# Performance work log

Hardware: AMD Instinct MI355X
Metric: run time of the kernel (lower is better)

Reference implementation:

```python
import jax, jax.numpy as jnp
import numpy as np


def setup_inputs() -> dict:
    key = jax.random.key(0)
    k_x, k_w1, k_w2 = jax.random.split(key, 3)
    b, d, m, h = 256, 2048, 64, 128  # batch, d_model, history_length, d_out
    lim1 = 1.0 / np.sqrt(m + h)
    lim2 = 1.0 / np.sqrt(h + d)
    x = jax.random.normal(k_x, (b, d, m), dtype=jnp.float32)
    w1 = jax.random.uniform(k_w1, (m, h, d), dtype=jnp.float32, minval=-lim1, maxval=lim1)
    b1 = jnp.zeros((1, h, d), dtype=jnp.float32)
    w2 = jax.random.uniform(k_w2, (h, d), dtype=jnp.float32, minval=-lim2, maxval=lim2)
    b2 = jnp.zeros((1, h), dtype=jnp.float32)
    return {"x": x, "w1": w1, "b1": b1, "w2": w2, "b2": b2}


def reference(x, w1, b1, w2, b2):
    # per-neuron (per-d) MLP: contract over history m, then over hidden h
    hidden = jnp.einsum('bdm,mhd->bhd', x, w1) + b1  # (b, h, d)
    out = jnp.einsum('bhd,hd->bh', hidden, w2) + b2  # (b, h)
    return out
```

## Files before the change

### kernel.cpp

```cpp
#include <hip/hip_runtime.h>

typedef unsigned short u16;
typedef __attribute__((ext_vector_type(8))) short short8;
typedef __attribute__((ext_vector_type(4))) float f32x4;

#define D_TOT 2048
#define M_TOT 64
#define H_TOT 128
#define B_TOT 256
#define NG    256
#define XB    131072
#define W1M   262144

__device__ __forceinline__ u16 f2bf(float f) {
  unsigned u = __builtin_bit_cast(unsigned, f);
  u = (u + 0x7fffu + ((u >> 16) & 1u)) >> 16;
  return (u16)u;
}
__device__ __forceinline__ float bf2f(u16 v) {
  unsigned u = ((unsigned)v) << 16;
  return __builtin_bit_cast(float, u);
}

__global__ __launch_bounds__(256)
void nlm_p0(const float* __restrict__ b1, const float* __restrict__ w2,
            const float* __restrict__ b2, float* __restrict__ ch) {
  const int h = blockIdx.x, t = threadIdx.x;
  const float4* pb = (const float4*)(b1 + (size_t)h * D_TOT);
  const float4* pw = (const float4*)(w2 + (size_t)h * D_TOT);
  float s = 0.f;
  for (int i = t; i < D_TOT / 4; i += 256) {
    float4 a = pb[i], w = pw[i];
    s += a.x * w.x + a.y * w.y + a.z * w.z + a.w * w.w;
  }
  __shared__ float red[256];
  red[t] = s;
  __syncthreads();
  for (int off = 128; off > 0; off >>= 1) {
    if (t < off) red[t] += red[t + off];
    __syncthreads();
  }
  if (t == 0) ch[h] = red[0] + b2[h];
}

__global__ __launch_bounds__(256)
void nlm_pw(const float* __restrict__ w1, const float* __restrict__ w2,
            u16* __restrict__ Bp) {
  const int gq  = blockIdx.x & 63;
  const int hb  = blockIdx.x >> 6;
  const int dq0 = gq * 32;
  const int t   = threadIdx.x;
  __shared__ u16 tile[32 * 16 * 64];

#pragma unroll
  for (int rep = 0; rep < 4; ++rep) {
    const int tau = rep * 256 + t;
    const int h_l = tau >> 6, m = tau & 63;
    const int h   = hb * 16 + h_l;
    const float* w1p = w1 + (size_t)m * W1M + (size_t)h * D_TOT + dq0;
    const float* w2p = w2 + (size_t)h * D_TOT + dq0;
    u16* dst = tile + h_l * 64 + m;
#pragma unroll
    for (int q = 0; q < 8; ++q) {
      float4 a = *(const float4*)(w1p + q * 4);
      float4 s = *(const float4*)(w2p + q * 4);
      dst[(q * 4 + 0) * 1024] = f2bf(a.x * s.x);
      dst[(q * 4 + 1) * 1024] = f2bf(a.y * s.y);
      dst[(q * 4 + 2) * 1024] = f2bf(a.z * s.z);
      dst[(q * 4 + 3) * 1024] = f2bf(a.w * s.w);
    }
  }
  __syncthreads();
#pragma unroll 4
  for (int dc = 0; dc < 32; ++dc) {
    const int g = gq * 4 + (dc >> 3), c = dc & 7;
    u16* out = Bp + (((size_t)g * 8 + c) * H_TOT + hb * 16) * 64 + t * 4;
    *(ushort4*)out = *(const ushort4*)(tile + dc * 1024 + t * 4);
  }
}

__global__ __launch_bounds__(512, 4)
void nlm_p1(const float* __restrict__ x, const u16* __restrict__ Bp,
            u16* __restrict__ partial) {
  __shared__ __align__(16) u16 As[64 * 72];
  __shared__ __align__(16) u16 Bs[128 * 72];

  const int tid  = threadIdx.x;
  const int g    = blockIdx.x & 255;
  const int bq   = blockIdx.x >> 8;
  const int d0   = g * 8;
  const int lane = tid & 63, wave = tid >> 6;
  const int wm   = wave >> 2;
  const int wn   = wave & 3;
  const int quad = lane >> 4, l16 = lane & 15;

  const int a_bl = tid >> 3, a_p = tid & 7;
  const float* xrow = x + (size_t)(bq * 64 + a_bl) * XB
                        + (size_t)d0 * M_TOT + a_p * 8;
  const int b_h = tid >> 2, b_qp = tid & 3;
  const u16* bsrc = Bp + ((size_t)g * 8 * H_TOT + b_h) * 64 + b_qp * 16;

  f32x4 acc[2][2];
#pragma unroll
  for (int i = 0; i < 2; ++i)
#pragma unroll
    for (int j = 0; j < 2; ++j) acc[i][j] = (f32x4){0.f, 0.f, 0.f, 0.f};

  for (int c = 0; c < 8; ++c) {
    {
      const float* xp = xrow + c * M_TOT;
      float4 v0 = *(const float4*)(xp);
      float4 v1 = *(const float4*)(xp + 4);
      short8 av;
      av[0] = (short)f2bf(v0.x); av[1] = (short)f2bf(v0.y);
      av[2] = (short)f2bf(v0.z); av[3] = (short)f2bf(v0.w);
      av[4] = (short)f2bf(v1.x); av[5] = (short)f2bf(v1.y);
      av[6] = (short)f2bf(v1.z); av[7] = (short)f2bf(v1.w);
      *(short8*)(As + a_bl * 72 + a_p * 8) = av;
    }
    {
      const u16* bp = bsrc + (size_t)c * (H_TOT * 64);
      *(short8*)(Bs + b_h * 72 + b_qp * 16)     = *(const short8*)(bp);
      *(short8*)(Bs + b_h * 72 + b_qp * 16 + 8) = *(const short8*)(bp + 8);
    }
    __syncthreads();
#pragma unroll
    for (int s = 0; s < 2; ++s) {
      short8 af[2], bf[2];
#pragma unroll
      for (int i = 0; i < 2; ++i)
        af[i] = *(const short8*)(As + (wm * 32 + i * 16 + l16) * 72 + s * 32 + quad * 8);
#pragma unroll
      for (int j = 0; j < 2; ++j)
        bf[j] = *(const short8*)(Bs + (wn * 32 + j * 16 + l16) * 72 + s * 32 + quad * 8);
#pragma unroll
      for (int i = 0; i < 2; ++i)
#pragma unroll
        for (int j = 0; j < 2; ++j)
          acc[i][j] = __builtin_amdgcn_mfma_f32_16x16x32_bf16(af[i], bf[j], acc[i][j], 0, 0, 0);
    }
    __syncthreads();
  }

#pragma unroll
  for (int i = 0; i < 2; ++i)
#pragma unroll
    for (int j = 0; j < 2; ++j) {
      const int hcol = wn * 32 + j * 16 + l16;
#pragma unroll
      for (int r = 0; r < 4; ++r) {
        const int brow = bq * 64 + wm * 32 + i * 16 + quad * 4 + r;
        partial[((size_t)brow * NG + g) * H_TOT + hcol] = f2bf(acc[i][j][r]);
      }
    }
}

__global__ __launch_bounds__(256)
void nlm_p2(const u16* __restrict__ partial, const float* __restrict__ ch,
            float* __restrict__ out) {
  const int b = blockIdx.x, t = threadIdx.x;
  const int h2   = t & 63;
  const int half = t >> 6;
  const u16* base = partial + ((size_t)b * NG + half * 64) * H_TOT + 2 * h2;
  float s0 = 0.f, s1 = 0.f;
#pragma unroll 8
  for (int gg = 0; gg < 64; ++gg) {
    unsigned v = __builtin_nontemporal_load((const unsigned*)(base + (size_t)gg * H_TOT));
    s0 += bf2f((u16)(v & 0xffffu));
    s1 += bf2f((u16)(v >> 16));
  }
  __shared__ float red0[256], red1[256];
  red0[t] = s0;
  red1[t] = s1;
  __syncthreads();
  if (t < 64) {
    float a0 = red0[t] + red0[t + 64] + red0[t + 128] + red0[t + 192];
    float a1 = red1[t] + red1[t + 64] + red1[t + 128] + red1[t + 192];
    out[(size_t)b * H_TOT + 2 * t]     = a0 + ch[2 * t];
    out[(size_t)b * H_TOT + 2 * t + 1] = a1 + ch[2 * t + 1];
  }
}

extern "C" void kernel_launch(void* const* d_in, const int* in_sizes, int n_in,
                              void* d_out, int out_size, void* d_ws, size_t ws_size,
                              hipStream_t stream) {
  const float* x  = (const float*)d_in[0];
  const float* w1 = (const float*)d_in[1];
  const float* b1 = (const float*)d_in[2];
  const float* w2 = (const float*)d_in[3];
  const float* b2 = (const float*)d_in[4];
  float* out = (float*)d_out;

  u16*   partial = (u16*)d_ws;
  u16*   Bp      = (u16*)((char*)d_ws + (size_t)B_TOT * NG * H_TOT * sizeof(u16));
  float* ch      = (float*)((char*)d_ws + (size_t)B_TOT * NG * H_TOT * sizeof(u16)
                                        + (size_t)NG * 8 * H_TOT * 64 * sizeof(u16));

  nlm_p0<<<dim3(128),  dim3(256), 0, stream>>>(b1, w2, b2, ch);
  nlm_pw<<<dim3(512),  dim3(256), 0, stream>>>(w1, w2, Bp);
  nlm_p1<<<dim3(1024), dim3(512), 0, stream>>>(x, Bp, partial);
  nlm_p2<<<dim3(256),  dim3(256), 0, stream>>>(partial, ch, out);
}
```

Before: 266.8 us.

## Double-group d per block and prefetch next chunk into registers

Each p1 block now covers 16 d-values instead of 8, which halves the grid and halves the bf16 partial-sum buffer written by p1 and read back by p2. The global loads for the next chunk of x and Bp are issued into registers right after the barrier, so they overlap with the MFMA work on the current chunk. The Bp layout is simplified to a flat per-d index. The cost is fewer blocks (512) to fill the GPU and more registers held live per thread.

Measured after the change: 273.9 us. 2.6% more time.

```diff
diff --git a/kernel.cpp b/kernel.cpp
--- a/kernel.cpp
+++ b/kernel.cpp
@@ -8,7 +8,7 @@
 #define M_TOT 64
 #define H_TOT 128
 #define B_TOT 256
-#define NG    256
+#define NGRP  128
 #define XB    131072
 #define W1M   262144
 
@@ -73,8 +73,8 @@
   __syncthreads();
 #pragma unroll 4
   for (int dc = 0; dc < 32; ++dc) {
-    const int g = gq * 4 + (dc >> 3), c = dc & 7;
-    u16* out = Bp + (((size_t)g * 8 + c) * H_TOT + hb * 16) * 64 + t * 4;
+    const int dg = dq0 + dc;
+    u16* out = Bp + ((size_t)dg * H_TOT + hb * 16) * 64 + t * 4;
     *(ushort4*)out = *(const ushort4*)(tile + dc * 1024 + t * 4);
   }
 }
@@ -86,9 +86,9 @@
   __shared__ __align__(16) u16 Bs[128 * 72];
 
   const int tid  = threadIdx.x;
-  const int g    = blockIdx.x & 255;
-  const int bq   = blockIdx.x >> 8;
-  const int d0   = g * 8;
+  const int G    = blockIdx.x & 127;
+  const int bq   = blockIdx.x >> 7;
+  const int dg0  = G * 16;
   const int lane = tid & 63, wave = tid >> 6;
   const int wm   = wave >> 2;
   const int wn   = wave & 3;
@@ -96,9 +96,9 @@
 
   const int a_bl = tid >> 3, a_p = tid & 7;
   const float* xrow = x + (size_t)(bq * 64 + a_bl) * XB
-                        + (size_t)d0 * M_TOT + a_p * 8;
+                        + (size_t)dg0 * M_TOT + a_p * 8;
   const int b_h = tid >> 2, b_qp = tid & 3;
-  const u16* bsrc = Bp + ((size_t)g * 8 * H_TOT + b_h) * 64 + b_qp * 16;
+  const u16* bsrc = Bp + ((size_t)dg0 * H_TOT + b_h) * 64 + b_qp * 16;
 
   f32x4 acc[2][2];
 #pragma unroll
@@ -106,24 +106,35 @@
 #pragma unroll
     for (int j = 0; j < 2; ++j) acc[i][j] = (f32x4){0.f, 0.f, 0.f, 0.f};
 
-  for (int c = 0; c < 8; ++c) {
+  float4 xv0, xv1; short8 bv0, bv1;
+  {
+    const float* xp = xrow;
+    xv0 = *(const float4*)(xp);
+    xv1 = *(const float4*)(xp + 4);
+    bv0 = *(const short8*)(bsrc);
+    bv1 = *(const short8*)(bsrc + 8);
+  }
+
+  for (int c = 0; c < 16; ++c) {
     {
-      const float* xp = xrow + c * M_TOT;
-      float4 v0 = *(const float4*)(xp);
-      float4 v1 = *(const float4*)(xp + 4);
       short8 av;
-      av[0] = (short)f2bf(v0.x); av[1] = (short)f2bf(v0.y);
-      av[2] = (short)f2bf(v0.z); av[3] = (short)f2bf(v0.w);
-      av[4] = (short)f2bf(v1.x); av[5] = (short)f2bf(v1.y);
-      av[6] = (short)f2bf(v1.z); av[7] = (short)f2bf(v1.w);
+      av[0] = (short)f2bf(xv0.x); av[1] = (short)f2bf(xv0.y);
+      av[2] = (short)f2bf(xv0.z); av[3] = (short)f2bf(xv0.w);
+      av[4] = (short)f2bf(xv1.x); av[5] = (short)f2bf(xv1.y);
+      av[6] = (short)f2bf(xv1.z); av[7] = (short)f2bf(xv1.w);
       *(short8*)(As + a_bl * 72 + a_p * 8) = av;
-    }
-    {
-      const u16* bp = bsrc + (size_t)c * (H_TOT * 64);
-      *(short8*)(Bs + b_h * 72 + b_qp * 16)     = *(const short8*)(bp);
-      *(short8*)(Bs + b_h * 72 + b_qp * 16 + 8) = *(const short8*)(bp + 8);
+      *(short8*)(Bs + b_h * 72 + b_qp * 16)     = bv0;
+      *(short8*)(Bs + b_h * 72 + b_qp * 16 + 8) = bv1;
     }
     __syncthreads();
+    if (c < 15) {
+      const float* xp = xrow + (c + 1) * M_TOT;
+      xv0 = *(const float4*)(xp);
+      xv1 = *(const float4*)(xp + 4);
+      const u16* bp = bsrc + (size_t)(c + 1) * (H_TOT * 64);
+      bv0 = *(const short8*)(bp);
+      bv1 = *(const short8*)(bp + 8);
+    }
 #pragma unroll
     for (int s = 0; s < 2; ++s) {
       short8 af[2], bf[2];
@@ -150,7 +161,7 @@
 #pragma unroll
       for (int r = 0; r < 4; ++r) {
         const int brow = bq * 64 + wm * 32 + i * 16 + quad * 4 + r;
-        partial[((size_t)brow * NG + g) * H_TOT + hcol] = f2bf(acc[i][j][r]);
+        partial[((size_t)brow * NGRP + G) * H_TOT + hcol] = f2bf(acc[i][j][r]);
       }
     }
 }
@@ -160,11 +171,11 @@
             float* __restrict__ out) {
   const int b = blockIdx.x, t = threadIdx.x;
   const int h2   = t & 63;
-  const int half = t >> 6;
-  const u16* base = partial + ((size_t)b * NG + half * 64) * H_TOT + 2 * h2;
+  const int qtr  = t >> 6;
+  const u16* base = partial + ((size_t)b * NGRP + qtr * 32) * H_TOT + 2 * h2;
   float s0 = 0.f, s1 = 0.f;
 #pragma unroll 8
-  for (int gg = 0; gg < 64; ++gg) {
+  for (int gg = 0; gg < 32; ++gg) {
     unsigned v = __builtin_nontemporal_load((const unsigned*)(base + (size_t)gg * H_TOT));
     s0 += bf2f((u16)(v & 0xffffu));
     s1 += bf2f((u16)(v >> 16));
@@ -192,12 +203,12 @@
   float* out = (float*)d_out;
 
   u16*   partial = (u16*)d_ws;
-  u16*   Bp      = (u16*)((char*)d_ws + (size_t)B_TOT * NG * H_TOT * sizeof(u16));
-  float* ch      = (float*)((char*)d_ws + (size_t)B_TOT * NG * H_TOT * sizeof(u16)
-                                        + (size_t)NG * 8 * H_TOT * 64 * sizeof(u16));
+  u16*   Bp      = (u16*)((char*)d_ws + (size_t)B_TOT * NGRP * H_TOT * sizeof(u16));
+  float* ch      = (float*)((char*)d_ws + (size_t)B_TOT * NGRP * H_TOT * sizeof(u16)
+                                        + (size_t)D_TOT * H_TOT * 64 * sizeof(u16));
 
   nlm_p0<<<dim3(128),  dim3(256), 0, stream>>>(b1, w2, b2, ch);
   nlm_pw<<<dim3(512),  dim3(256), 0, stream>>>(w1, w2, Bp);
-  nlm_p1<<<dim3(1024), dim3(512), 0, stream>>>(x, Bp, partial);
+  nlm_p1<<<dim3(512),  dim3(512), 0, stream>>>(x, Bp, partial);
   nlm_p2<<<dim3(256),  dim3(256), 0, stream>>>(partial, ch, out);
 }
```
